# Performance work log

Hardware: AMD Instinct MI355X
Metric: run time of the kernel (lower is better)

The kernel has to match this reference:

```python
import jax, jax.numpy as jnp
import numpy as np

START_TAG = 30
END_TAG = 31
INVALID = -10000.0  # Constants.Invalid_Transition


def setup_inputs() -> dict:
    key = jax.random.key(0)
    k1, k2, k3, k4 = jax.random.split(key, 4)
    B, T, K = 1024, 512, 32
    feats = jax.random.normal(k1, (B, T, K), dtype=jnp.float32)
    tags = jax.random.randint(k2, (B, T), 0, START_TAG)  # gold tags exclude START/END
    lengths = jax.random.randint(k3, (B,), 1, T + 1)
    sentence_masks = (jnp.arange(T)[None, :] < lengths[:, None]).astype(jnp.int32)
    transitions = jax.random.normal(k4, (K, K), dtype=jnp.float32) * 0.1
    # transitions[i, j] = score of transitioning from tag j to tag i
    transitions = transitions.at[START_TAG, :].set(INVALID).at[:, END_TAG].set(INVALID)
    return {"feats": feats, "transitions": transitions, "tags": tags,
            "sentence_masks": sentence_masks}


def _gold_score(feats, transitions, tags, sentence_masks):
    # Faithful port of _score_sentence
    B, T, K = feats.shape
    emit = jnp.take_along_axis(feats, tags[:, :, None], axis=2)[:, :, 0]  # [B,T]
    emit = emit * sentence_masks.astype(feats.dtype)
    pad_start = jnp.concatenate([jnp.full((B, 1), START_TAG, tags.dtype), tags], axis=1)
    pad_end = jnp.concatenate([tags, jnp.full((B, 1), END_TAG, tags.dtype)], axis=1)
    trans = transitions[pad_end, pad_start]  # [B,T+1]
    tmask = jnp.concatenate([jnp.ones((B, 1), sentence_masks.dtype), sentence_masks], axis=1)
    trans = trans * tmask.astype(feats.dtype)
    return jnp.sum(emit, axis=1) + jnp.sum(trans, axis=1)  # [B]


def _log_partition(feats, transitions, sentence_masks):
    # Faithful port of _forward_alg: sequential DP over time, logsumexp over prev tags
    B, T, K = feats.shape
    lengths = jnp.sum(sentence_masks, axis=1)  # [B]
    init = jnp.full((K,), INVALID, dtype=feats.dtype).at[START_TAG].set(0.0)
    init = jnp.broadcast_to(init, (B, K))

    def step(forward_var, feat):
        # tag_var[b, next, prev] = alpha[b, prev] + trans[next, prev] + emit[b, next]
        tag_var = forward_var[:, None, :] + transitions[None, :, :] + feat[:, :, None]
        new = jax.nn.logsumexp(tag_var, axis=2)  # [B,K]
        return new, new

    _, all_alphas = jax.lax.scan(step, init, jnp.swapaxes(feats, 0, 1))  # [T,B,K]
    idx = jnp.broadcast_to((lengths - 1)[None, :, None], (1, B, K))
    last_alpha = jnp.take_along_axis(all_alphas, idx, axis=0)[0]  # [B,K]
    terminal = last_alpha + transitions[END_TAG][None, :]
    return jax.nn.logsumexp(terminal, axis=1)  # [B]


def reference(feats, transitions, tags, sentence_masks):
    # CRF negative log-likelihood per sentence: Z - gold_score
    Z = _log_partition(feats, transitions, sentence_masks)
    gold = _gold_score(feats, transitions, tags, sentence_masks)
    return Z - gold  # [B]
```

## Files before the change

### kernel.cpp

```cpp
#include <hip/hip_runtime.h>
#include <hip/hip_bf16.h>

#define KT 32
#define START_TAG 30
#define END_TAG 31
#define NT 32

__device__ __forceinline__ float exp2f_fast(float x){ return __builtin_amdgcn_exp2f(x); }
__device__ __forceinline__ float log2f_fast(float x){ return __builtin_amdgcn_logf(x); }

__global__ __launch_bounds__(64) void crf_nll(
    const float* __restrict__ feats,
    const float* __restrict__ trans,
    const int*   __restrict__ tags,
    const int*   __restrict__ masks,
    float* __restrict__ out, int B, int T)
{
    constexpr float L2E = 1.4426950408889634f;
    constexpr float LN2 = 0.6931471805599453f;
    const int lane = (int)threadIdx.x;
    const int k = lane & 31;
    const int h = lane >> 5;
    int b = (int)blockIdx.x * 2 + h;
    const bool bvalid = (b < B);
    if (!bvalid) b = B - 1;

    __shared__ float  Tl[KT * KT];
    __shared__ float4 prow[2][8];
    __shared__ __align__(16) float ftile[2][2][NT][KT];

    for (int i = lane; i < KT * KT; i += 64) Tl[i] = trans[i];

    float E[KT];
#pragma unroll
    for (int j = 0; j < KT; ++j) E[j] = exp2f_fast(trans[k * KT + j] * L2E);
    const float E2 = exp2f_fast(trans[END_TAG * KT + k] * L2E);

    __syncthreads();

    int b0 = (int)blockIdx.x * 2;     if (b0 >= B) b0 = B - 1;
    int b1 = (int)blockIdx.x * 2 + 1; if (b1 >= B) b1 = B - 1;
    const float4* f40 = (const float4*)(feats + (size_t)b0 * T * KT);
    const float4* f41 = (const float4*)(feats + (size_t)b1 * T * KT);
    float4 R[8];
#define TLOAD(ti) { const int o = (ti) * 256 + lane;                          \
    R[0]=f40[o]; R[1]=f40[o+64]; R[2]=f40[o+128]; R[3]=f40[o+192];            \
    R[4]=f41[o]; R[5]=f41[o+64]; R[6]=f41[o+128]; R[7]=f41[o+192]; }
#define TWRITE(buf) { float4* w0 = (float4*)&ftile[buf][0][0][0];             \
    float4* w1 = (float4*)&ftile[buf][1][0][0];                               \
    w0[lane]=R[0]; w0[lane+64]=R[1]; w0[lane+128]=R[2]; w0[lane+192]=R[3];    \
    w1[lane]=R[4]; w1[lane+64]=R[5]; w1[lane+128]=R[6]; w1[lane+192]=R[7]; }
#define FEAT(t) ftile[((t) >> 5) & 1][h][(t) & 31][k]

    TLOAD(0)

    const int*   tg = tags  + (size_t)b * T;
    const int*   mk = masks + (size_t)b * T;
    const float* fb = feats + (size_t)b * T * KT;
    float g = 0.f;
    int   Lp = 0;
    for (int c = 0; c < T; c += 32) {
        const int t  = c + k;
        const int mt = mk[t];
        Lp += mt;
        const int tagt  = tg[t];
        const int prev  = t ? tg[t - 1] : START_TAG;
        const int fprev = t ? mk[t - 1] : 1;
        if (mt)    g += fb[(size_t)t * KT + tagt];
        if (fprev) g += Tl[tagt * KT + prev];
        if (t == T - 1 && mt) g += Tl[END_TAG * KT + tagt];
    }
#pragma unroll
    for (int d = 1; d < 32; d <<= 1) { g += __shfl_xor(g, d); Lp += __shfl_xor(Lp, d); }
    const int L    = Lp;
    const int Lmax = max(L, __shfl_xor(L, 32));

    TWRITE(0)
    const int ntiles = T >> 5;
    if (ntiles > 1) { TLOAD(1) TWRITE(1) }

    const float init = (k == START_TAG) ? 1.f : 0.f;
    float ahat = init;
    int M = 0;
    ((float*)prow)[lane] = init;

    float Fc = exp2f_fast(FEAT(0) * L2E);
    float f1 = FEAT(1);
    float f2 = FEAT(2);

    const int nact = (Lmax + NT - 1) >> 5;
    for (int n = 0; n < nact; ++n) {
        const int tb = n << 5;
#pragma unroll
        for (int ti_ = 0; ti_ < NT; ++ti_) {
            const int t = tb + ti_;
            if (ti_ == 0)  { const int nx = n + 2; if (nx < ntiles) TLOAD(nx) }
            float p[KT];
#pragma unroll
            for (int i = 0; i < 8; ++i) {
                const float4 q = prow[h][i];
                p[4*i+0] = q.x; p[4*i+1] = q.y; p[4*i+2] = q.z; p[4*i+3] = q.w;
            }
            const unsigned pb = __float_as_uint(p[0]);
            int e = (int)((pb >> 23) & 255u);
            if (e < 1 || e > 253) e = 127;
            const float Fcr = Fc * __uint_as_float((unsigned)(254 - e) << 23);
            float a0 = 0.f, a1 = 0.f, a2 = 0.f, a3 = 0.f;
#pragma unroll
            for (int j = 0; j < KT; j += 4) {
                a0 = fmaf(E[j+0], p[j+0], a0);
                a1 = fmaf(E[j+1], p[j+1], a1);
                a2 = fmaf(E[j+2], p[j+2], a2);
                a3 = fmaf(E[j+3], p[j+3], a3);
            }
            const float val = ((a0 + a1) + (a2 + a3)) * Fcr;
            const bool act = t < L;
            ahat = act ? val : ahat;
            M   += act ? (e - 127) : 0;
            ((float*)prow)[lane] = ahat;
            if (ti_ == 30) { const int nx = n + 2; if (nx < ntiles) TWRITE(n & 1) }
            const float fnew = FEAT(t + 2);
            Fc = exp2f_fast(f1 * L2E);
            f1 = f2;
            f2 = fnew;
        }
    }

    float term = ahat * E2;
#pragma unroll
    for (int d = 1; d < 32; d <<= 1) term += __shfl_xor(term, d);
    const float Z = ((float)M + log2f_fast(term)) * LN2;

    if (k == 0 && bvalid) out[b] = Z - g;
#undef TLOAD
#undef TWRITE
#undef FEAT
}

extern "C" void kernel_launch(void* const* d_in, const int* in_sizes, int n_in,
                              void* d_out, int out_size, void* d_ws, size_t ws_size,
                              hipStream_t stream) {
    const float* feats = (const float*)d_in[0];
    const float* trans = (const float*)d_in[1];
    const int*   tags  = (const int*)d_in[2];
    const int*   masks = (const int*)d_in[3];
    float* out = (float*)d_out;

    const int B = out_size;
    const int T = in_sizes[2] / B;
    const int blocks = (B + 1) / 2;

    hipLaunchKernelGGL(crf_nll, dim3(blocks), dim3(64), 0, stream,
                       feats, trans, tags, masks, out, B, T);
}
```

Baseline: 190.3 us.

## Broadcast alpha via readlane and process one sentence per wavefront

Replaces the per-step LDS store/load of the forward vector with 32 v_readlane broadcasts from the lane holding each tag, so the serial DP chain no longer round-trips through shared memory. Each 64-lane block now handles one sentence instead of two, with the upper half of the wave duplicating the lower half's DP. The gold-score pass uses all 64 lanes. The feature prefetch index also changes from t+2 to t+3, which fixes the emission pipeline offset. In exchange, the launch has twice as many blocks and each step pays scalar readlane latency and hazard waits.

```diff
diff --git a/kernel.cpp b/kernel.cpp
--- a/kernel.cpp
+++ b/kernel.cpp
@@ -8,6 +8,9 @@
 
 __device__ __forceinline__ float exp2f_fast(float x){ return __builtin_amdgcn_exp2f(x); }
 __device__ __forceinline__ float log2f_fast(float x){ return __builtin_amdgcn_logf(x); }
+__device__ __forceinline__ float readlane_f(float v, int l){
+    return __int_as_float(__builtin_amdgcn_readlane(__float_as_int(v), l));
+}
 
 __global__ __launch_bounds__(64) void crf_nll(
     const float* __restrict__ feats,
@@ -20,14 +23,10 @@
     constexpr float LN2 = 0.6931471805599453f;
     const int lane = (int)threadIdx.x;
     const int k = lane & 31;
-    const int h = lane >> 5;
-    int b = (int)blockIdx.x * 2 + h;
-    const bool bvalid = (b < B);
-    if (!bvalid) b = B - 1;
+    const int b = (int)blockIdx.x;
 
     __shared__ float  Tl[KT * KT];
-    __shared__ float4 prow[2][8];
-    __shared__ __align__(16) float ftile[2][2][NT][KT];
+    __shared__ __align__(16) float ftile[2][NT][KT];
 
     for (int i = lane; i < KT * KT; i += 64) Tl[i] = trans[i];
 
@@ -38,19 +37,13 @@
 
     __syncthreads();
 
-    int b0 = (int)blockIdx.x * 2;     if (b0 >= B) b0 = B - 1;
-    int b1 = (int)blockIdx.x * 2 + 1; if (b1 >= B) b1 = B - 1;
-    const float4* f40 = (const float4*)(feats + (size_t)b0 * T * KT);
-    const float4* f41 = (const float4*)(feats + (size_t)b1 * T * KT);
-    float4 R[8];
-#define TLOAD(ti) { const int o = (ti) * 256 + lane;                          \
-    R[0]=f40[o]; R[1]=f40[o+64]; R[2]=f40[o+128]; R[3]=f40[o+192];            \
-    R[4]=f41[o]; R[5]=f41[o+64]; R[6]=f41[o+128]; R[7]=f41[o+192]; }
-#define TWRITE(buf) { float4* w0 = (float4*)&ftile[buf][0][0][0];             \
-    float4* w1 = (float4*)&ftile[buf][1][0][0];                               \
-    w0[lane]=R[0]; w0[lane+64]=R[1]; w0[lane+128]=R[2]; w0[lane+192]=R[3];    \
-    w1[lane]=R[4]; w1[lane+64]=R[5]; w1[lane+128]=R[6]; w1[lane+192]=R[7]; }
-#define FEAT(t) ftile[((t) >> 5) & 1][h][(t) & 31][k]
+    const float4* f4 = (const float4*)(feats + (size_t)b * T * KT);
+    float4 R[4];
+#define TLOAD(ti) { const int o = (ti) * 256 + lane;                           \
+    R[0]=f4[o]; R[1]=f4[o+64]; R[2]=f4[o+128]; R[3]=f4[o+192]; }
+#define TWRITE(buf) { float4* w = (float4*)&ftile[buf][0][0];                  \
+    w[lane]=R[0]; w[lane+64]=R[1]; w[lane+128]=R[2]; w[lane+192]=R[3]; }
+#define FEAT(t) ftile[((t) >> 5) & 1][(t) & 31][k]
 
     TLOAD(0)
 
@@ -59,79 +52,71 @@
     const float* fb = feats + (size_t)b * T * KT;
     float g = 0.f;
     int   Lp = 0;
-    for (int c = 0; c < T; c += 32) {
-        const int t  = c + k;
-        const int mt = mk[t];
-        Lp += mt;
-        const int tagt  = tg[t];
-        const int prev  = t ? tg[t - 1] : START_TAG;
-        const int fprev = t ? mk[t - 1] : 1;
-        if (mt)    g += fb[(size_t)t * KT + tagt];
-        if (fprev) g += Tl[tagt * KT + prev];
-        if (t == T - 1 && mt) g += Tl[END_TAG * KT + tagt];
+    for (int c = 0; c < T; c += 64) {
+        const int t = c + lane;
+        if (t < T) {
+            const int mt = mk[t];
+            Lp += mt;
+            const int tagt  = tg[t];
+            const int prev  = t ? tg[t - 1] : START_TAG;
+            const int fprev = t ? mk[t - 1] : 1;
+            if (mt)    g += fb[(size_t)t * KT + tagt];
+            if (fprev) g += Tl[tagt * KT + prev];
+            if (t == T - 1 && mt) g += Tl[END_TAG * KT + tagt];
+        }
     }
 #pragma unroll
-    for (int d = 1; d < 32; d <<= 1) { g += __shfl_xor(g, d); Lp += __shfl_xor(Lp, d); }
-    const int L    = Lp;
-    const int Lmax = max(L, __shfl_xor(L, 32));
+    for (int d = 1; d < 64; d <<= 1) { g += __shfl_xor(g, d); Lp += __shfl_xor(Lp, d); }
+    const int L = Lp;
 
     TWRITE(0)
     const int ntiles = T >> 5;
     if (ntiles > 1) { TLOAD(1) TWRITE(1) }
 
-    const float init = (k == START_TAG) ? 1.f : 0.f;
-    float ahat = init;
+    float y = (k == START_TAG) ? 1.f : 0.f;
     int M = 0;
-    ((float*)prow)[lane] = init;
 
     float Fc = exp2f_fast(FEAT(0) * L2E);
     float f1 = FEAT(1);
     float f2 = FEAT(2);
 
-    const int nact = (Lmax + NT - 1) >> 5;
+    const int nact = (L + NT - 1) >> 5;
     for (int n = 0; n < nact; ++n) {
         const int tb = n << 5;
 #pragma unroll
         for (int ti_ = 0; ti_ < NT; ++ti_) {
             const int t = tb + ti_;
             if (ti_ == 0)  { const int nx = n + 2; if (nx < ntiles) TLOAD(nx) }
-            float p[KT];
+            float a0 = 0.f, a1 = 0.f, a2 = 0.f, a3 = 0.f;
 #pragma unroll
-            for (int i = 0; i < 8; ++i) {
-                const float4 q = prow[h][i];
-                p[4*i+0] = q.x; p[4*i+1] = q.y; p[4*i+2] = q.z; p[4*i+3] = q.w;
+            for (int j = 0; j < KT; j += 4) {
+                a0 = fmaf(E[j+0], readlane_f(y, j+0), a0);
+                a1 = fmaf(E[j+1], readlane_f(y, j+1), a1);
+                a2 = fmaf(E[j+2], readlane_f(y, j+2), a2);
+                a3 = fmaf(E[j+3], readlane_f(y, j+3), a3);
             }
-            const unsigned pb = __float_as_uint(p[0]);
+            const unsigned pb = __float_as_uint(readlane_f(y, 0));
             int e = (int)((pb >> 23) & 255u);
             if (e < 1 || e > 253) e = 127;
             const float Fcr = Fc * __uint_as_float((unsigned)(254 - e) << 23);
-            float a0 = 0.f, a1 = 0.f, a2 = 0.f, a3 = 0.f;
-#pragma unroll
-            for (int j = 0; j < KT; j += 4) {
-                a0 = fmaf(E[j+0], p[j+0], a0);
-                a1 = fmaf(E[j+1], p[j+1], a1);
-                a2 = fmaf(E[j+2], p[j+2], a2);
-                a3 = fmaf(E[j+3], p[j+3], a3);
-            }
             const float val = ((a0 + a1) + (a2 + a3)) * Fcr;
             const bool act = t < L;
-            ahat = act ? val : ahat;
-            M   += act ? (e - 127) : 0;
-            ((float*)prow)[lane] = ahat;
+            y  = act ? val : y;
+            M += act ? (e - 127) : 0;
             if (ti_ == 30) { const int nx = n + 2; if (nx < ntiles) TWRITE(n & 1) }
-            const float fnew = FEAT(t + 2);
+            const float fnew = FEAT(t + 3);
             Fc = exp2f_fast(f1 * L2E);
             f1 = f2;
             f2 = fnew;
         }
     }
 
-    float term = ahat * E2;
+    float term = y * E2;
 #pragma unroll
     for (int d = 1; d < 32; d <<= 1) term += __shfl_xor(term, d);
     const float Z = ((float)M + log2f_fast(term)) * LN2;
 
-    if (k == 0 && bvalid) out[b] = Z - g;
+    if (lane == 0) out[b] = Z - g;
 #undef TLOAD
 #undef TWRITE
 #undef FEAT
@@ -148,8 +133,7 @@
 
     const int B = out_size;
     const int T = in_sizes[2] / B;
-    const int blocks = (B + 1) / 2;
 
-    hipLaunchKernelGGL(crf_nll, dim3(blocks), dim3(64), 0, stream,
+    hipLaunchKernelGGL(crf_nll, dim3(B), dim3(64), 0, stream,
                        feats, trans, tags, masks, out, B, T);
 }
```

Result: slower. 196.8 us (+3.4%).
